# Kernel optimization log

Hardware: AMD Instinct MI355X
Metric: run time of the kernel (lower is better)

## Reference

```python
import jax, jax.numpy as jnp
import numpy as np

IB = 8; WB = 8; ABMVM = 8; ABNM = 8; N_MSB = 4; NL = 0.0  # noise_level=0 -> deterministic
B = 4096; IN = 1024; H = 1024

sg = jax.lax.stop_gradient

def quant_raw(x, bits, r):
    step = 2.0 ** (bits - 1)
    xs = jnp.clip(x / r, -1.0 + 1.0 / step, 1.0 - 1.0 / step)
    return jnp.round(xs * step) / step * r

def quant_ste(x, bits, r):
    # straight-through: value = quantized, grad = identity wrt x, no grad to r
    return x + sg(quant_raw(x, bits, r) - x)

def pact(x, a):
    # sign(x)*0.5*(|x| - ||x|-a| + a) == clamp(x, -a, a), kept literal for fidelity
    return jnp.sign(x) * 0.5 * (jnp.abs(x) - jnp.abs(jnp.abs(x) - a) + a)

def bitsplit(x, bits, n_msb):
    # symmetric bit-splitting; STE backward: each y_i has identity grad wrt x
    ste = x - sg(x)
    xv = sg(x)
    beta = 1.0
    ys = []
    for _ in range(n_msb):
        y = quant_raw(xv / beta, bits, 1.0)
        xv = xv - y * beta
        ys.append(y + ste)
        beta = beta / 2.0
    betas = jnp.asarray([1.0 / (2.0 ** i) for i in range(n_msb)], dtype=x.dtype)
    return jnp.stack(ys), betas  # [n_msb, B, D], [n_msb]

def custom_mm(inp, w, b, key):
    # forward: inp @ (quant(clamp(w)) + noise) + quant(b) + noise
    # backward (torch custom): grads use RAW w/b -> STE via out_lin path
    kw, kb = jax.random.split(key)
    n = inp.shape[0]
    noise_w = jax.random.normal(kw, (n, w.shape[1], w.shape[2]), dtype=w.dtype) * NL
    noise_b = jax.random.normal(kb, (n, 1, b.shape[2]), dtype=b.dtype) * NL
    wq = quant_raw(jnp.clip(w, -1.0, 1.0), WB, 1.0)
    bq = quant_raw(b, WB, 1.0)
    out_val = jnp.einsum('nbi,nio->nbo', inp, wq + noise_w) + (bq + noise_b)
    out_lin = jnp.einsum('nbi,io->nbo', inp, w[0]) + b
    return out_lin + sg(out_val - out_lin)

def _cell(input, hx, cx, weight_ih, weight_hh, bias_ih, bias_hh,
          a1, a3, a4, a5, a6, a7, a8, a9, a10, a11):
    k1, k2 = jax.random.split(jax.random.key(42))
    ys, betas = bitsplit(pact(input, a1) / a1, IB, N_MSB)
    out_q = quant_ste(custom_mm(ys, weight_ih, bias_ih, k1), ABMVM, 1.0)
    part1 = (betas[:, None, None] * out_q).sum(0) * a1          # [B, 4H]
    ys, betas = bitsplit(pact(hx, a11) / a11, IB, N_MSB)
    out_q = quant_ste(custom_mm(ys, weight_hh, bias_hh, k2), ABMVM, 1.0)
    part2 = (betas[:, None, None] * out_q).sum(0) * a11
    gates = part1 + part2
    i, j, f, o = jnp.split(gates, 4, axis=1)
    fg = quant_ste(pact(jax.nn.sigmoid(f), a3), ABNM, a3)
    ig = quant_ste(pact(jax.nn.sigmoid(i), a4), ABNM, a4)
    act = quant_ste(pact(jnp.tanh(j), a5), ABNM, a5)
    og = quant_ste(pact(jax.nn.sigmoid(o), a6), ABNM, a6)
    gc = quant_ste(pact(cx * fg, a7), ABNM, a7)
    ai = quant_ste(pact(ig * act, a8), ABNM, a8)
    new_c = quant_ste(pact(gc + ai, a9), ABNM, a9)
    ac = quant_ste(pact(jnp.tanh(new_c), a10), ABNM, a10)
    new_h = quant_ste(pact(ac * og, a11), ABNM, a11)
    return jnp.stack([new_h, new_c])  # [2, B, H]

def setup_inputs() -> dict:
    key = jax.random.key(0)
    ks = jax.random.split(key, 7)
    return {
        'input': jax.random.normal(ks[0], (B, IN), dtype=jnp.float32),
        'hx': jax.random.normal(ks[1], (B, H), dtype=jnp.float32),
        'cx': jax.random.normal(ks[2], (B, H), dtype=jnp.float32),
        'weight_ih': jax.random.normal(ks[3], (1, IN, 4 * H), dtype=jnp.float32) * 0.05,
        'weight_hh': jax.random.normal(ks[4], (1, H, 4 * H), dtype=jnp.float32) * 0.05,
        'bias_ih': jax.random.normal(ks[5], (1, 1, 4 * H), dtype=jnp.float32) * 0.05,
        'bias_hh': jax.random.normal(ks[6], (1, 1, 4 * H), dtype=jnp.float32) * 0.05,
        'a1': jnp.array([128.0]), 'a3': jnp.array([1.0]), 'a4': jnp.array([1.0]),
        'a5': jnp.array([1.0]), 'a6': jnp.array([1.0]), 'a7': jnp.array([4.0]),
        'a8': jnp.array([1.0]), 'a9': jnp.array([4.0]), 'a10': jnp.array([1.0]),
        'a11': jnp.array([4.0]),
    }

def reference(input, hx, cx, weight_ih, weight_hh, bias_ih, bias_hh,
              a1, a3, a4, a5, a6, a7, a8, a9, a10, a11):
    return _cell(input, hx, cx, weight_ih, weight_hh, bias_ih, bias_hh,
                 a1, a3, a4, a5, a6, a7, a8, a9, a10, a11)
```

## Files before the change

### kernel.cpp

```cpp
#include <hip/hip_runtime.h>
#include <cstdint>

typedef unsigned short u16;
typedef __attribute__((ext_vector_type(4))) int i32x4;

#define DEVI __device__ __forceinline__

DEVI float pactf(float x, float a) {
    float ax = fabsf(x);
    float w  = fabsf(ax - a);
    float t  = (ax - w) + a;
    float s  = (x > 0.f) ? 0.5f : ((x < 0.f) ? -0.5f : 0.0f);
    return s * t;
}
DEVI float quantf(float x, float r) {
    float xs = x / r;
    xs = fminf(fmaxf(xs, -0.9921875f), 0.9921875f);
    float e = rintf(xs * 128.0f);
    return (e * 0.0078125f) * r;
}
DEVI float sigf(float x) {
    float eg  = (float)exp(-(double)x);
    float den = 1.0f + eg;
    return 1.0f / den;
}
DEVI float tanf32(float x) { return (float)tanh((double)x); }

#define KSIG  4436
#define NSIG  8873
#define KTANH 2309
#define NTANH 4619

DEVI float sig_lut(float g, const float* __restrict__ Ts) {
    float g256 = g * 256.0f;
    float kf = rintf(g256);
    if (kf == g256) {
        if (kf >  (float)KSIG) return 1.0f;
        if (kf < -(float)KSIG) return 0.0f;
        return Ts[(int)kf + KSIG];
    }
    return sigf(g);
}
DEVI float tanh_lut(float g, const float* __restrict__ Tt) {
    float g256 = g * 256.0f;
    float kf = rintf(g256);
    if (kf == g256) {
        if (fabsf(kf) <= (float)KTANH) return Tt[(int)kf + KTANH];
        return copysignf(1.0f, g);
    }
    return tanf32(g);
}

__global__ void prep_misc(const float* __restrict__ b0, const float* __restrict__ b1,
                          float* __restrict__ Bf, float* __restrict__ Ts,
                          float* __restrict__ Tt) {
    int i = blockIdx.x * 256 + threadIdx.x;
    if (i < NSIG)  Ts[i] = sigf((float)(i - KSIG)  * 0.00390625f);
    if (i < NTANH) Tt[i] = tanf32((float)(i - KTANH) * 0.00390625f);
    if (i < 8192) {
        const float* b = (i < 4096) ? b0 : b1;
        float v = b[i & 4095];
        float xs = fminf(fmaxf(v, -0.9921875f), 0.9921875f);
        Bf[i] = rintf(xs * 128.f);
    }
}

__global__ void prep_act2(const float* __restrict__ X0, const float* __restrict__ X1,
                          const float* __restrict__ a1p, const float* __restrict__ a11p,
                          signed char* __restrict__ A) {
    int blk = blockIdx.x;
    int lo = (blk < 4096) ? 1 : 0;
    const float* X = lo ? X0 : X1;
    float a = lo ? a1p[0] : a11p[0];
    int planebase = lo ? 0 : 4;
    int idx4 = ((blk & 4095) * 256 + threadIdx.x) * 4;
    float4 xv4 = *(const float4*)(X + idx4);
    float v[4] = {xv4.x, xv4.y, xv4.z, xv4.w};
    signed char e4[4][4];
#pragma unroll
    for (int el = 0; el < 4; el++) {
        float x = pactf(v[el], a) / a;
        float xv = x;
        float beta = 1.0f;
#pragma unroll
        for (int n = 0; n < 4; n++) {
            float xs = xv / beta;
            xs = fminf(fmaxf(xs, -0.9921875f), 0.9921875f);
            float e = rintf(xs * 128.0f);
            e4[n][el] = (signed char)(int)e;
            float y = e * 0.0078125f;
            xv = xv - y * beta;
            beta = beta * 0.5f;
        }
    }
#pragma unroll
    for (int n = 0; n < 4; n++)
        *(char4*)(A + (size_t)(planebase + n) * 4194304u + idx4) =
            make_char4(e4[n][0], e4[n][1], e4[n][2], e4[n][3]);
}

__global__ void prep_w(const float* __restrict__ W0, const float* __restrict__ W1,
                       signed char* __restrict__ Wt) {
    __shared__ float tile[32][33];
    int proj = blockIdx.z;
    const float* W = proj ? W1 : W0;
    int n0 = blockIdx.x * 32, k0 = blockIdx.y * 32;
    int tx = threadIdx.x, ty = threadIdx.y;
#pragma unroll
    for (int i = 0; i < 4; i++)
        tile[ty + i * 8][tx] = W[(size_t)(k0 + ty + i * 8) * 4096 + n0 + tx];
    __syncthreads();
#pragma unroll
    for (int i = 0; i < 4; i++) {
        float w = tile[tx][ty + i * 8];
        float xs = fminf(fmaxf(w, -0.9921875f), 0.9921875f);
        float e = rintf(xs * 128.f);
        Wt[(size_t)proj * 4194304u + (size_t)(n0 + ty + i * 8) * 1024 + k0 + tx] =
            (signed char)(int)e;
    }
}

#define GLOAD16(gp, lp) __builtin_amdgcn_global_load_lds( \
    (const __attribute__((address_space(1))) void*)(gp),  \
    (__attribute__((address_space(3))) void*)(lp), 16, 0, 0)

__global__ __launch_bounds__(256) void gemm_planes(
    const signed char* __restrict__ A, const signed char* __restrict__ Wt,
    const float* __restrict__ Bf, signed char* __restrict__ E) {
    __shared__ __align__(16) signed char lds[32768];
    int tid = threadIdx.x;
    int c0 = blockIdx.x * 128;
    int r0 = blockIdx.y * 128;
    int proj = (r0 >= 16384) ? 1 : 0;

    int srow = tid >> 2;
    int g16  = (((tid & 3) + 4 - ((tid >> 3) & 3)) & 3) * 16;
    const signed char* gA = A + (size_t)(r0 + srow) * 1024 + g16;
    const signed char* gB = Wt + (size_t)proj * 4194304u + (size_t)(c0 + srow) * 1024 + g16;

    int w = tid >> 6, l = tid & 63;
    int wm = (w >> 1) * 64, wn = (w & 1) * 64;
    int quad = l >> 4, lrow = l & 15;

    int stoff = tid * 16;
    int slot  = ((quad + (lrow >> 1)) & 3) * 16;
    int fAoff = (wm + lrow) * 64 + slot;
    int fBoff = 8192 + (wn + lrow) * 64 + slot;

    i32x4 acc[4][4] = {};

#define STAGE(bufbase)                                        \
    do {                                                      \
        signed char* lb = lds + (bufbase) + stoff;            \
        GLOAD16(gA,             lb);                          \
        GLOAD16(gA + 64 * 1024, lb + 4096);                   \
        GLOAD16(gB,             lb + 8192);                   \
        GLOAD16(gB + 64 * 1024, lb + 12288);                  \
        gA += 64; gB += 64;                                   \
    } while (0)

#define COMPUTE(bufbase)                                      \
    do {                                                      \
        const signed char* fA = lds + (bufbase) + fAoff;      \
        const signed char* fB = lds + (bufbase) + fBoff;      \
        i32x4 af[4], bfr[4];                                  \
        _Pragma("unroll")                                     \
        for (int mt = 0; mt < 4; mt++) af[mt] = *(const i32x4*)(fA + mt * 1024);  \
        _Pragma("unroll")                                     \
        for (int nt = 0; nt < 4; nt++) bfr[nt] = *(const i32x4*)(fB + nt * 1024); \
        _Pragma("unroll")                                     \
        for (int mt = 0; mt < 4; mt++)                        \
            _Pragma("unroll")                                 \
            for (int nt = 0; nt < 4; nt++)                    \
                acc[mt][nt] = __builtin_amdgcn_mfma_i32_16x16x64_i8( \
                    af[mt], bfr[nt], acc[mt][nt], 0, 0, 0);   \
    } while (0)

    STAGE(0);
    asm volatile("s_waitcnt vmcnt(0)" ::: "memory");
    __syncthreads();

    for (int k0 = 0; k0 < 1024; k0 += 128) {
        STAGE(16384);
        COMPUTE(0);
        __syncthreads();
        if (k0 + 128 < 1024) STAGE(0);
        COMPUTE(16384);
        __syncthreads();
    }
#undef STAGE
#undef COMPUTE

    signed char* ctile = lds;
#pragma unroll
    for (int nt = 0; nt < 4; nt++) {
        int lc = wn + nt * 16 + lrow;
        float bb = Bf[proj * 4096 + c0 + lc];
#pragma unroll
        for (int mt = 0; mt < 4; mt++) {
            int lr = wm + mt * 16 + quad * 4;
#pragma unroll
            for (int r = 0; r < 4; r++) {
                float t = (float)acc[mt][nt][r] * 0.0078125f + bb;
                float tc = fminf(fmaxf(t, -127.f), 127.f);
                ctile[(lr + r) * 144 + lc] = (signed char)(int)rintf(tc);
            }
        }
    }
    __syncthreads();
#pragma unroll
    for (int p = 0; p < 4; p++) {
        int lr = (tid >> 3) + p * 32;
        int lc = (tid & 7) * 16;
        *(int4*)(E + (size_t)(r0 + lr) * 4096 + c0 + lc) =
            *(const int4*)(ctile + lr * 144 + lc);
    }
}

__global__ __launch_bounds__(256) void gates_kernel_t(
    const signed char* __restrict__ E, const float* __restrict__ cx,
    float* __restrict__ out,
    const float* __restrict__ Ts, const float* __restrict__ Tt,
    const float* __restrict__ a1p, const float* __restrict__ a3p,
    const float* __restrict__ a4p, const float* __restrict__ a5p,
    const float* __restrict__ a6p, const float* __restrict__ a7p,
    const float* __restrict__ a8p, const float* __restrict__ a9p,
    const float* __restrict__ a10p, const float* __restrict__ a11p) {
    int tid = threadIdx.x;
    int b = blockIdx.x;
    int h0 = tid * 4;
    float a1 = a1p[0], a3 = a3p[0], a4 = a4p[0], a5 = a5p[0], a6 = a6p[0];
    float a7 = a7p[0], a8 = a8p[0], a9 = a9p[0], a10 = a10p[0], a11 = a11p[0];

    float gate[4][4];
#pragma unroll
    for (int g = 0; g < 4; g++) {
        size_t colbase = (size_t)g * 1024 + h0;
        int s1[4] = {0, 0, 0, 0}, s2[4] = {0, 0, 0, 0};
#pragma unroll
        for (int n = 0; n < 4; n++) {
            char4 e1 = *(const char4*)(E + (((size_t)(n * 4096 + b)) << 12) + colbase);
            char4 e2 = *(const char4*)(E + (((size_t)((4 + n) * 4096 + b)) << 12) + colbase);
            int wgt = 8 >> n;
            s1[0] += (int)e1.x * wgt; s1[1] += (int)e1.y * wgt;
            s1[2] += (int)e1.z * wgt; s1[3] += (int)e1.w * wgt;
            s2[0] += (int)e2.x * wgt; s2[1] += (int)e2.y * wgt;
            s2[2] += (int)e2.z * wgt; s2[3] += (int)e2.w * wgt;
        }
#pragma unroll
        for (int jj = 0; jj < 4; jj++) {
            float p1 = ((float)s1[jj] * 0.0009765625f) * a1;
            float p2 = ((float)s2[jj] * 0.0009765625f) * a11;
            gate[g][jj] = p1 + p2;
        }
    }

    float4 cxv = *(const float4*)(cx + (size_t)b * 1024 + h0);
    float cxa[4] = {cxv.x, cxv.y, cxv.z, cxv.w};
    float nh[4], ncv[4];
#pragma unroll
    for (int jj = 0; jj < 4; jj++) {
        float gi = gate[0][jj], gj = gate[1][jj], gf = gate[2][jj], go = gate[3][jj];
        float fg  = quantf(pactf(sig_lut(gf, Ts), a3), a3);
        float ig  = quantf(pactf(sig_lut(gi, Ts), a4), a4);
        float act = quantf(pactf(tanh_lut(gj, Tt), a5), a5);
        float og  = quantf(pactf(sig_lut(go, Ts), a6), a6);
        float gc  = quantf(pactf(cxa[jj] * fg, a7), a7);
        float ai  = quantf(pactf(ig * act, a8), a8);
        float nc  = quantf(pactf(gc + ai, a9), a9);
        float ac  = quantf(pactf(tanh_lut(nc, Tt), a10), a10);
        float hh  = quantf(pactf(ac * og, a11), a11);
        nh[jj]  = hh;
        ncv[jj] = nc;
    }
    float4 o1 = {nh[0], nh[1], nh[2], nh[3]};
    float4 o2 = {ncv[0], ncv[1], ncv[2], ncv[3]};
    *(float4*)(out + (size_t)b * 1024 + h0) = o1;
    *(float4*)(out + 4194304u + (size_t)b * 1024 + h0) = o2;
}

extern "C" void kernel_launch(void* const* d_in, const int* in_sizes, int n_in,
                              void* d_out, int out_size, void* d_ws, size_t ws_size,
                              hipStream_t stream) {
    const float* input = (const float*)d_in[0];
    const float* hx    = (const float*)d_in[1];
    const float* cx    = (const float*)d_in[2];
    const float* wih   = (const float*)d_in[3];
    const float* whh   = (const float*)d_in[4];
    const float* bih   = (const float*)d_in[5];
    const float* bhh   = (const float*)d_in[6];
    const float* a1  = (const float*)d_in[7];
    const float* a3  = (const float*)d_in[8];
    const float* a4  = (const float*)d_in[9];
    const float* a5  = (const float*)d_in[10];
    const float* a6  = (const float*)d_in[11];
    const float* a7  = (const float*)d_in[12];
    const float* a8  = (const float*)d_in[13];
    const float* a9  = (const float*)d_in[14];
    const float* a10 = (const float*)d_in[15];
    const float* a11 = (const float*)d_in[16];

    char* ws = (char*)d_ws;
    signed char* A  = (signed char*)ws;
    signed char* Wt = (signed char*)(ws + 33554432);
    float*       Bf = (float*)(ws + 41943040);
    float*       Ts = (float*)(ws + 41975808);
    float*       Tt = (float*)(ws + 42011300);
    signed char* E  = (signed char*)(ws + 42041344);

    prep_misc<<<35, 256, 0, stream>>>(bih, bhh, Bf, Ts, Tt);
    prep_act2<<<8192, 256, 0, stream>>>(input, hx, a1, a11, A);
    prep_w<<<dim3(128, 32, 2), dim3(32, 8), 0, stream>>>(wih, whh, Wt);
    gemm_planes<<<dim3(32, 256), 256, 0, stream>>>(A, Wt, Bf, E);
    gates_kernel_t<<<4096, 256, 0, stream>>>(E, cx, (float*)d_out, Ts, Tt,
                                             a1, a3, a4, a5, a6, a7, a8, a9, a10, a11);
}
```

Measured before the change: 373.0 us.

## Fuse int8 plane GEMM with LSTM gate epilogue via permuted gate columns

Weight rows and biases are permuted so that each 128-column output tile holds all four gates for 32 hidden units. One GEMM block now loops over all 8 bit-planes, folds each plane's requantized result into packed 16-bit register accumulators, then runs the gate nonlinearities and writes h and c directly. This removes the large intermediate E tensor and its round trip through memory, and drops the separate gates kernel launch. The costs are a larger LDS footprint, 512-thread blocks, and more register pressure for the packed accumulators.

```diff
diff --git a/kernel.cpp b/kernel.cpp
--- a/kernel.cpp
+++ b/kernel.cpp
@@ -58,10 +58,12 @@
     if (i < NSIG)  Ts[i] = sigf((float)(i - KSIG)  * 0.00390625f);
     if (i < NTANH) Tt[i] = tanf32((float)(i - KTANH) * 0.00390625f);
     if (i < 8192) {
-        const float* b = (i < 4096) ? b0 : b1;
-        float v = b[i & 4095];
+        int proj = i >> 12, nn = i & 4095;
+        const float* b = proj ? b1 : b0;
+        float v = b[nn];
         float xs = fminf(fmaxf(v, -0.9921875f), 0.9921875f);
-        Bf[i] = rintf(xs * 128.f);
+        int np_ = ((nn & 1023) << 2) | (nn >> 10);
+        Bf[proj * 4096 + np_] = rintf(xs * 128.f);
     }
 }
 
@@ -112,10 +114,12 @@
     __syncthreads();
 #pragma unroll
     for (int i = 0; i < 4; i++) {
+        int nn = n0 + ty + i * 8;
         float w = tile[tx][ty + i * 8];
         float xs = fminf(fmaxf(w, -0.9921875f), 0.9921875f);
         float e = rintf(xs * 128.f);
-        Wt[(size_t)proj * 4194304u + (size_t)(n0 + ty + i * 8) * 1024 + k0 + tx] =
+        int np_ = ((nn & 1023) << 2) | (nn >> 10);
+        Wt[(size_t)proj * 4194304u + (size_t)np_ * 1024 + k0 + tx] =
             (signed char)(int)e;
     }
 }
@@ -124,101 +128,9 @@
     (const __attribute__((address_space(1))) void*)(gp),  \
     (__attribute__((address_space(3))) void*)(lp), 16, 0, 0)
 
-__global__ __launch_bounds__(256) void gemm_planes(
+__global__ __launch_bounds__(512, 4) void gemm_fused(
     const signed char* __restrict__ A, const signed char* __restrict__ Wt,
-    const float* __restrict__ Bf, signed char* __restrict__ E) {
-    __shared__ __align__(16) signed char lds[32768];
-    int tid = threadIdx.x;
-    int c0 = blockIdx.x * 128;
-    int r0 = blockIdx.y * 128;
-    int proj = (r0 >= 16384) ? 1 : 0;
-
-    int srow = tid >> 2;
-    int g16  = (((tid & 3) + 4 - ((tid >> 3) & 3)) & 3) * 16;
-    const signed char* gA = A + (size_t)(r0 + srow) * 1024 + g16;
-    const signed char* gB = Wt + (size_t)proj * 4194304u + (size_t)(c0 + srow) * 1024 + g16;
-
-    int w = tid >> 6, l = tid & 63;
-    int wm = (w >> 1) * 64, wn = (w & 1) * 64;
-    int quad = l >> 4, lrow = l & 15;
-
-    int stoff = tid * 16;
-    int slot  = ((quad + (lrow >> 1)) & 3) * 16;
-    int fAoff = (wm + lrow) * 64 + slot;
-    int fBoff = 8192 + (wn + lrow) * 64 + slot;
-
-    i32x4 acc[4][4] = {};
-
-#define STAGE(bufbase)                                        \
-    do {                                                      \
-        signed char* lb = lds + (bufbase) + stoff;            \
-        GLOAD16(gA,             lb);                          \
-        GLOAD16(gA + 64 * 1024, lb + 4096);                   \
-        GLOAD16(gB,             lb + 8192);                   \
-        GLOAD16(gB + 64 * 1024, lb + 12288);                  \
-        gA += 64; gB += 64;                                   \
-    } while (0)
-
-#define COMPUTE(bufbase)                                      \
-    do {                                                      \
-        const signed char* fA = lds + (bufbase) + fAoff;      \
-        const signed char* fB = lds + (bufbase) + fBoff;      \
-        i32x4 af[4], bfr[4];                                  \
-        _Pragma("unroll")                                     \
-        for (int mt = 0; mt < 4; mt++) af[mt] = *(const i32x4*)(fA + mt * 1024);  \
-        _Pragma("unroll")                                     \
-        for (int nt = 0; nt < 4; nt++) bfr[nt] = *(const i32x4*)(fB + nt * 1024); \
-        _Pragma("unroll")                                     \
-        for (int mt = 0; mt < 4; mt++)                        \
-            _Pragma("unroll")                                 \
-            for (int nt = 0; nt < 4; nt++)                    \
-                acc[mt][nt] = __builtin_amdgcn_mfma_i32_16x16x64_i8( \
-                    af[mt], bfr[nt], acc[mt][nt], 0, 0, 0);   \
-    } while (0)
-
-    STAGE(0);
-    asm volatile("s_waitcnt vmcnt(0)" ::: "memory");
-    __syncthreads();
-
-    for (int k0 = 0; k0 < 1024; k0 += 128) {
-        STAGE(16384);
-        COMPUTE(0);
-        __syncthreads();
-        if (k0 + 128 < 1024) STAGE(0);
-        COMPUTE(16384);
-        __syncthreads();
-    }
-#undef STAGE
-#undef COMPUTE
-
-    signed char* ctile = lds;
-#pragma unroll
-    for (int nt = 0; nt < 4; nt++) {
-        int lc = wn + nt * 16 + lrow;
-        float bb = Bf[proj * 4096 + c0 + lc];
-#pragma unroll
-        for (int mt = 0; mt < 4; mt++) {
-            int lr = wm + mt * 16 + quad * 4;
-#pragma unroll
-            for (int r = 0; r < 4; r++) {
-                float t = (float)acc[mt][nt][r] * 0.0078125f + bb;
-                float tc = fminf(fmaxf(t, -127.f), 127.f);
-                ctile[(lr + r) * 144 + lc] = (signed char)(int)rintf(tc);
-            }
-        }
-    }
-    __syncthreads();
-#pragma unroll
-    for (int p = 0; p < 4; p++) {
-        int lr = (tid >> 3) + p * 32;
-        int lc = (tid & 7) * 16;
-        *(int4*)(E + (size_t)(r0 + lr) * 4096 + c0 + lc) =
-            *(const int4*)(ctile + lr * 144 + lc);
-    }
-}
-
-__global__ __launch_bounds__(256) void gates_kernel_t(
-    const signed char* __restrict__ E, const float* __restrict__ cx,
+    const float* __restrict__ Bf, const float* __restrict__ cx,
     float* __restrict__ out,
     const float* __restrict__ Ts, const float* __restrict__ Tt,
     const float* __restrict__ a1p, const float* __restrict__ a3p,
@@ -226,57 +138,151 @@
     const float* __restrict__ a6p, const float* __restrict__ a7p,
     const float* __restrict__ a8p, const float* __restrict__ a9p,
     const float* __restrict__ a10p, const float* __restrict__ a11p) {
+    __shared__ __align__(16) signed char lds[67584];
     int tid = threadIdx.x;
-    int b = blockIdx.x;
-    int h0 = tid * 4;
-    float a1 = a1p[0], a3 = a3p[0], a4 = a4p[0], a5 = a5p[0], a6 = a6p[0];
-    float a7 = a7p[0], a8 = a8p[0], a9 = a9p[0], a10 = a10p[0], a11 = a11p[0];
-
-    float gate[4][4];
-#pragma unroll
-    for (int g = 0; g < 4; g++) {
-        size_t colbase = (size_t)g * 1024 + h0;
-        int s1[4] = {0, 0, 0, 0}, s2[4] = {0, 0, 0, 0};
-#pragma unroll
-        for (int n = 0; n < 4; n++) {
-            char4 e1 = *(const char4*)(E + (((size_t)(n * 4096 + b)) << 12) + colbase);
-            char4 e2 = *(const char4*)(E + (((size_t)((4 + n) * 4096 + b)) << 12) + colbase);
-            int wgt = 8 >> n;
-            s1[0] += (int)e1.x * wgt; s1[1] += (int)e1.y * wgt;
-            s1[2] += (int)e1.z * wgt; s1[3] += (int)e1.w * wgt;
-            s2[0] += (int)e2.x * wgt; s2[1] += (int)e2.y * wgt;
-            s2[2] += (int)e2.z * wgt; s2[3] += (int)e2.w * wgt;
-        }
-#pragma unroll
-        for (int jj = 0; jj < 4; jj++) {
-            float p1 = ((float)s1[jj] * 0.0009765625f) * a1;
-            float p2 = ((float)s2[jj] * 0.0009765625f) * a11;
-            gate[g][jj] = p1 + p2;
-        }
-    }
-
-    float4 cxv = *(const float4*)(cx + (size_t)b * 1024 + h0);
-    float cxa[4] = {cxv.x, cxv.y, cxv.z, cxv.w};
-    float nh[4], ncv[4];
-#pragma unroll
-    for (int jj = 0; jj < 4; jj++) {
-        float gi = gate[0][jj], gj = gate[1][jj], gf = gate[2][jj], go = gate[3][jj];
+    int c0 = blockIdx.x * 128;
+    int b0 = blockIdx.y * 128;
+
+    int srow = tid >> 2;
+    int g16  = (((tid & 3) + 4 - ((tid >> 3) & 3)) & 3) * 16;
+    const signed char* Ab = A + (size_t)(b0 + srow) * 1024 + g16;
+    const signed char* Bb = Wt + (size_t)(c0 + srow) * 1024 + g16;
+
+    int w = tid >> 6, l = tid & 63;
+    int wm = (w >> 1) * 32, wn = (w & 1) * 64;
+    int quad = l >> 4, lrow = l & 15;
+
+    int stoff = tid * 16;
+    int slot  = ((quad + (lrow >> 1)) & 3) * 16;
+    int fAoff = (wm + lrow) * 64 + slot;
+    int fBoff = 8192 + (wn + lrow) * 64 + slot;
+
+    float biasA[4], biasB[4];
+#pragma unroll
+    for (int nt = 0; nt < 4; nt++) {
+        int col = c0 + wn + nt * 16 + lrow;
+        biasA[nt] = Bf[col];
+        biasB[nt] = Bf[4096 + col];
+    }
+
+    i32x4 acc[2][4] = {};
+    i32x4 packed[2][4];
+#pragma unroll
+    for (int mt = 0; mt < 2; mt++)
+#pragma unroll
+        for (int nt = 0; nt < 4; nt++)
+            packed[mt][nt] = (i32x4){0x08000800, 0x08000800, 0x08000800, 0x08000800};
+
+#define STAGE(bufbase, ts)                                              \
+    do {                                                                \
+        size_t ao = ((size_t)((ts) >> 4) << 22) + (size_t)(((ts) & 15) << 6); \
+        size_t bo = (((ts) >= 64) ? (size_t)4194304u : 0) + (size_t)(((ts) & 15) << 6); \
+        signed char* lb = lds + (bufbase) + stoff;                      \
+        GLOAD16(Ab + ao, lb);                                           \
+        GLOAD16(Bb + bo, lb + 8192);                                    \
+    } while (0)
+
+#define COMPUTE(bufbase)                                                \
+    do {                                                                \
+        const signed char* fA = lds + (bufbase) + fAoff;                \
+        const signed char* fB = lds + (bufbase) + fBoff;                \
+        i32x4 af[2], bfr[4];                                            \
+        _Pragma("unroll")                                               \
+        for (int mt = 0; mt < 2; mt++) af[mt] = *(const i32x4*)(fA + mt * 1024); \
+        _Pragma("unroll")                                               \
+        for (int nt = 0; nt < 4; nt++) bfr[nt] = *(const i32x4*)(fB + nt * 1024); \
+        _Pragma("unroll")                                               \
+        for (int mt = 0; mt < 2; mt++)                                  \
+            _Pragma("unroll")                                           \
+            for (int nt = 0; nt < 4; nt++)                              \
+                acc[mt][nt] = __builtin_amdgcn_mfma_i32_16x16x64_i8(    \
+                    af[mt], bfr[nt], acc[mt][nt], 0, 0, 0);             \
+    } while (0)
+
+#define FOLD(plane)                                                     \
+    do {                                                                \
+        int wgt = 8 >> ((plane) & 3);                                   \
+        int mulw = ((plane) < 4) ? wgt : (wgt << 16);                   \
+        _Pragma("unroll")                                               \
+        for (int mt = 0; mt < 2; mt++)                                  \
+            _Pragma("unroll")                                           \
+            for (int nt = 0; nt < 4; nt++) {                            \
+                float bb = ((plane) < 4) ? biasA[nt] : biasB[nt];       \
+                _Pragma("unroll")                                       \
+                for (int r = 0; r < 4; r++) {                           \
+                    float t = (float)acc[mt][nt][r] * 0.0078125f + bb;  \
+                    float tc = fminf(fmaxf(t, -127.f), 127.f);          \
+                    packed[mt][nt][r] += mulw * (int)rintf(tc);         \
+                    acc[mt][nt][r] = 0;                                 \
+                }                                                       \
+            }                                                           \
+    } while (0)
+
+    STAGE(0, 0);
+    asm volatile("s_waitcnt vmcnt(0)" ::: "memory");
+    __syncthreads();
+
+    for (int it = 0; it < 64; ++it) {
+        STAGE(16384, 2 * it + 1);
+        COMPUTE(0);
+        __syncthreads();
+        if (it < 63) STAGE(0, 2 * it + 2);
+        COMPUTE(16384);
+        if ((it & 7) == 7) FOLD(it >> 3);
+        __syncthreads();
+    }
+#undef STAGE
+#undef COMPUTE
+#undef FOLD
+
+    float a1v = a1p[0], a11v = a11p[0];
+#pragma unroll
+    for (int mt = 0; mt < 2; mt++)
+#pragma unroll
+        for (int nt = 0; nt < 4; nt++)
+#pragma unroll
+            for (int r = 0; r < 4; r++) {
+                int row = wm + mt * 16 + quad * 4 + r;
+                int col = wn + nt * 16 + lrow;
+                int pk = packed[mt][nt][r];
+                int s1 = (pk & 0xFFFF) - 2048;
+                int s2 = (pk >> 16) - 2048;
+                float gate = ((float)s1 * 0.0009765625f) * a1v +
+                             ((float)s2 * 0.0009765625f) * a11v;
+                *(float*)(lds + row * 528 + col * 4) = gate;
+            }
+    __syncthreads();
+
+    float a3 = a3p[0], a4 = a4p[0], a5 = a5p[0], a6 = a6p[0], a7 = a7p[0];
+    float a8 = a8p[0], a9 = a9p[0], a10 = a10p[0], a11 = a11p[0];
+
+    int row = tid >> 2;
+    int hc  = (tid & 3) * 8;
+    size_t obase = (size_t)(b0 + row) * 1024 + (c0 >> 2) + hc;
+    float4 cx0 = *(const float4*)(cx + obase);
+    float4 cx1 = *(const float4*)(cx + obase + 4);
+    float cxa[8] = {cx0.x, cx0.y, cx0.z, cx0.w, cx1.x, cx1.y, cx1.z, cx1.w};
+    float nh[8], ncv[8];
+#pragma unroll
+    for (int j = 0; j < 8; j++) {
+        float4 g4 = *(const float4*)(lds + row * 528 + (hc + j) * 16);
+        float gi = g4.x, gj = g4.y, gf = g4.z, go = g4.w;
         float fg  = quantf(pactf(sig_lut(gf, Ts), a3), a3);
         float ig  = quantf(pactf(sig_lut(gi, Ts), a4), a4);
         float act = quantf(pactf(tanh_lut(gj, Tt), a5), a5);
         float og  = quantf(pactf(sig_lut(go, Ts), a6), a6);
-        float gc  = quantf(pactf(cxa[jj] * fg, a7), a7);
+        float gc  = quantf(pactf(cxa[j] * fg, a7), a7);
         float ai  = quantf(pactf(ig * act, a8), a8);
         float nc  = quantf(pactf(gc + ai, a9), a9);
         float ac  = quantf(pactf(tanh_lut(nc, Tt), a10), a10);
         float hh  = quantf(pactf(ac * og, a11), a11);
-        nh[jj]  = hh;
-        ncv[jj] = nc;
-    }
-    float4 o1 = {nh[0], nh[1], nh[2], nh[3]};
-    float4 o2 = {ncv[0], ncv[1], ncv[2], ncv[3]};
-    *(float4*)(out + (size_t)b * 1024 + h0) = o1;
-    *(float4*)(out + 4194304u + (size_t)b * 1024 + h0) = o2;
+        nh[j]  = hh;
+        ncv[j] = nc;
+    }
+    *(float4*)(out + obase)                 = (float4){nh[0], nh[1], nh[2], nh[3]};
+    *(float4*)(out + obase + 4)             = (float4){nh[4], nh[5], nh[6], nh[7]};
+    *(float4*)(out + 4194304u + obase)      = (float4){ncv[0], ncv[1], ncv[2], ncv[3]};
+    *(float4*)(out + 4194304u + obase + 4)  = (float4){ncv[4], ncv[5], ncv[6], ncv[7]};
 }
 
 extern "C" void kernel_launch(void* const* d_in, const int* in_sizes, int n_in,
@@ -306,12 +312,11 @@
     float*       Bf = (float*)(ws + 41943040);
     float*       Ts = (float*)(ws + 41975808);
     float*       Tt = (float*)(ws + 42011300);
-    signed char* E  = (signed char*)(ws + 42041344);
 
     prep_misc<<<35, 256, 0, stream>>>(bih, bhh, Bf, Ts, Tt);
     prep_act2<<<8192, 256, 0, stream>>>(input, hx, a1, a11, A);
     prep_w<<<dim3(128, 32, 2), dim3(32, 8), 0, stream>>>(wih, whh, Wt);
-    gemm_planes<<<dim3(32, 256), 256, 0, stream>>>(A, Wt, Bf, E);
-    gates_kernel_t<<<4096, 256, 0, stream>>>(E, cx, (float*)d_out, Ts, Tt,
-                                             a1, a3, a4, a5, a6, a7, a8, a9, a10, a11);
-}
+    gemm_fused<<<dim3(32, 32), 512, 0, stream>>>(A, Wt, Bf, cx, (float*)d_out,
+                                                 Ts, Tt, a1, a3, a4, a5, a6,
+                                                 a7, a8, a9, a10, a11);
+}
```

Measured after the change: 334.7 us. 10.3% less time.
